# Performance work log

Measured on AMD Instinct MI355X. Metric: run time of the kernel, lower is better.

The kernel has to match this reference:

```python
import jax, jax.numpy as jnp
import numpy as np

B, T, E, H, V = 64, 512, 512, 512, 50000

def setup_inputs() -> dict:
    key = jax.random.key(0)
    ks = jax.random.split(key, 8)
    x = jax.random.randint(ks[0], (B, T), 0, V)
    h0 = jax.random.normal(ks[1], (B, H), jnp.float32) * 0.1
    c0 = jax.random.normal(ks[2], (B, H), jnp.float32) * 0.1
    emb = jax.random.normal(ks[3], (V, E), jnp.float32) * 0.02
    emb = emb.at[0].set(0.0)  # padding_idx=0
    s_i = 1.0 / np.sqrt(H)
    W_ih = jax.random.uniform(ks[4], (4 * H, E), jnp.float32, -s_i, s_i)
    W_hh = jax.random.uniform(ks[5], (4 * H, H), jnp.float32, -s_i, s_i)
    b_ih = jax.random.uniform(ks[6], (4 * H,), jnp.float32, -s_i, s_i)
    b_hh = jax.random.uniform(ks[7], (4 * H,), jnp.float32, -s_i, s_i)
    return {"x": x, "h0": h0, "c0": c0, "emb": emb,
            "W_ih": W_ih, "W_hh": W_hh, "b_ih": b_ih, "b_hh": b_hh}

def reference(x, h0, c0, emb, W_ih, W_hh, b_ih, b_hh):
    # embedding lookup (option 'a'): [B, T, E]
    xs = emb[x]
    # precompute input-to-gate projections for all timesteps: [B, T, 4H]
    pre = jnp.einsum('bte,ge->btg', xs, W_ih) + b_ih + b_hh
    pre_t = jnp.swapaxes(pre, 0, 1)  # [T, B, 4H]

    def step(carry, p_t):
        h, c = carry
        gates = p_t + h @ W_hh.T  # [B, 4H]
        i, f, g, o = jnp.split(gates, 4, axis=-1)
        i = jax.nn.sigmoid(i)
        f = jax.nn.sigmoid(f)
        g = jnp.tanh(g)
        o = jax.nn.sigmoid(o)
        c_new = f * c + i * g
        h_new = o * jnp.tanh(c_new)
        return (h_new, c_new), h_new

    _, hs = jax.lax.scan(step, (h0, c0), pre_t)  # hs: [T, B, H]
    # original stacks per-batch lists of per-timestep hidden states -> [B, T, H]
    return jnp.swapaxes(hs, 0, 1)
```

## Files before the change

kernel.cpp:

```cpp
#include <hip/hip_runtime.h>
#include <stdint.h>

typedef __attribute__((ext_vector_type(8))) short short8;
typedef __attribute__((ext_vector_type(4))) short short4_;
typedef __attribute__((ext_vector_type(4))) float f4;
typedef __attribute__((ext_vector_type(4))) uint32_t u32x4;

#define B_ 64
#define T_ 512
#define E_ 512
#define H_ 512
#define GH 2048

static __device__ __forceinline__ uint16_t f2bf(float f) {
  uint32_t u = __builtin_bit_cast(uint32_t, f);
  uint32_t r = (u + 0x7FFFu + ((u >> 16) & 1u)) >> 16;
  return (uint16_t)r;
}
static __device__ __forceinline__ float bf2f(uint16_t b) {
  return __builtin_bit_cast(float, (uint32_t)b << 16);
}
static __device__ __forceinline__ float sigmoidf_(float x) {
  return 1.0f / (1.0f + __expf(-x));
}
static __device__ __forceinline__ float tanhf_(float x) {
  float e = __expf(-2.0f * fabsf(x));
  float t = (1.0f - e) / (1.0f + e);
  return __builtin_copysignf(t, x);
}

static __device__ __forceinline__ u32x4 ld_flag4_cc(const int* p) {
  u32x4 v;
  asm volatile("global_load_dwordx4 %0, %1, off sc0 sc1\n\ts_waitcnt vmcnt(0)"
               : "=v"(v) : "v"(p) : "memory");
  return v;
}
static __device__ __forceinline__ void ld_x4_cc(u32x4* d, const void* p) {
  asm volatile("global_load_dwordx4 %0, %1, off sc0 sc1" : "=v"(*d) : "v"(p));
}
static __device__ __forceinline__ void st_u32_cc(uint32_t* p, uint32_t v) {
  asm volatile("global_store_dword %0, %1, off sc0 sc1" :: "v"(p), "v"(v) : "memory");
}
static __device__ __forceinline__ void st_flag_cc(int* p, int v) {
  asm volatile("global_store_dword %0, %1, off sc0 sc1" :: "v"(p), "v"(v) : "memory");
}

__global__ void k_prep(const float* __restrict__ Whh, uint16_t* __restrict__ Whi_g,
                       uint16_t* __restrict__ Wlo_g) {
  int i = blockIdx.x * 256 + threadIdx.x;
  float w = Whh[i];
  uint16_t hi = f2bf(w);
  Whi_g[i] = hi;
  Wlo_g[i] = f2bf(w - bf2f(hi));
}

__global__ void k_init(const float* __restrict__ h0, uint32_t* __restrict__ hP0,
                       int* __restrict__ flags) {
  int i = blockIdx.x * 256 + threadIdx.x;
  if (i < B_ * H_) {
    float v = h0[i];
    uint16_t hi = f2bf(v);
    uint16_t lo = f2bf(v - bf2f(hi));
    hP0[i] = (uint32_t)hi | ((uint32_t)lo << 16);
  }
  if (i < 128) flags[i] = 0;
}

__launch_bounds__(256)
__global__ void k_pre(const int* __restrict__ x, const float* __restrict__ emb,
                      const float* __restrict__ Wih, const float* __restrict__ bih,
                      const float* __restrict__ bhh, float* __restrict__ pre2, int t0) {
  __shared__ uint16_t As[128 * 64];
  __shared__ uint16_t Bs[128 * 64];
  const int tid = threadIdx.x;
  const int tm = blockIdx.x >> 4;
  const int tn = blockIdx.x & 15;
  const int wid = tid >> 6, lane = tid & 63;
  const int wr = wid >> 1, wc = wid & 1;

  const int arow = tid >> 1;
  const int half = tid & 1;
  const int m = tm * 128 + arow;
  const int bb = m & 63;
  const int tt = t0 + (m >> 6);
  const int xid = x[bb * T_ + tt];
  const float* asrc = emb + (size_t)xid * E_ + half * 32;
  const float* bsrc = Wih + (size_t)(tn * 128 + arow) * E_ + half * 32;

  f4 acc[4][4];
#pragma unroll
  for (int a = 0; a < 4; ++a)
#pragma unroll
    for (int b = 0; b < 4; ++b) acc[a][b] = (f4){0.f, 0.f, 0.f, 0.f};

  for (int kk = 0; kk < 8; ++kk) {
    __syncthreads();
#pragma unroll
    for (int gi = 0; gi < 4; ++gi) {
      f4 a0 = *(const f4*)(asrc + kk * 64 + gi * 8);
      f4 a1 = *(const f4*)(asrc + kk * 64 + gi * 8 + 4);
      f4 b0 = *(const f4*)(bsrc + kk * 64 + gi * 8);
      f4 b1 = *(const f4*)(bsrc + kk * 64 + gi * 8 + 4);
      short8 va, vb;
#pragma unroll
      for (int j = 0; j < 4; ++j) {
        va[j] = (short)f2bf(a0[j]); va[4 + j] = (short)f2bf(a1[j]);
        vb[j] = (short)f2bf(b0[j]); vb[4 + j] = (short)f2bf(b1[j]);
      }
      int kq = half * 4 + gi;
      *(short8*)(As + arow * 64 + (kq ^ (arow & 7)) * 8) = va;
      *(short8*)(Bs + arow * 64 + (kq ^ (arow & 7)) * 8) = vb;
    }
    __syncthreads();
#pragma unroll
    for (int ks = 0; ks < 2; ++ks) {
      short8 af[4], bfr[4];
#pragma unroll
      for (int mi = 0; mi < 4; ++mi) {
        int row = wr * 64 + mi * 16 + (lane & 15);
        int kq = ks * 4 + (lane >> 4);
        af[mi] = *(const short8*)(As + row * 64 + (kq ^ (row & 7)) * 8);
      }
#pragma unroll
      for (int ni = 0; ni < 4; ++ni) {
        int row = wc * 64 + ni * 16 + (lane & 15);
        int kq = ks * 4 + (lane >> 4);
        bfr[ni] = *(const short8*)(Bs + row * 64 + (kq ^ (row & 7)) * 8);
      }
#pragma unroll
      for (int mi = 0; mi < 4; ++mi)
#pragma unroll
        for (int ni = 0; ni < 4; ++ni)
          acc[mi][ni] = __builtin_amdgcn_mfma_f32_16x16x32_bf16(af[mi], bfr[ni], acc[mi][ni], 0, 0, 0);
    }
  }
#pragma unroll
  for (int ni = 0; ni < 4; ++ni) {
    int n = tn * 128 + wc * 64 + ni * 16 + (lane & 15);
    float bias = bih[n] + bhh[n];
    int q = n >> 9, u = n & 511;
    int ug = u >> 4, uloc = u & 15;
    int gl = q * 16 + uloc;
#pragma unroll
    for (int mi = 0; mi < 4; ++mi) {
      int mrow = tm * 128 + wr * 64 + mi * 16 + (lane >> 4) * 4;
      int trel = mrow >> 6;
      int bbr = mrow & 63;
      f4 vst;
#pragma unroll
      for (int j = 0; j < 4; ++j) vst[j] = acc[mi][ni][j] + bias;
      float* dst = pre2 + (((size_t)trel * 32 + ug) * 4 + (bbr >> 4)) * 1024 + gl * 16 + (bbr & 15);
      *(f4*)dst = vst;
    }
  }
}

__launch_bounds__(256)
__global__ void k_lstm(const float* __restrict__ pre2, const uint16_t* __restrict__ Whi_g,
                       const uint16_t* __restrict__ Wlo_g, const float* __restrict__ c0,
                       float* __restrict__ out, uint32_t* __restrict__ hP0,
                       uint32_t* __restrict__ hP1, float* __restrict__ c_state,
                       int* __restrict__ flags, int t0, int TB) {
  extern __shared__ char smem[];
  uint16_t* WhiL = (uint16_t*)smem;
  uint16_t* WloL = (uint16_t*)(smem + 65536);
  uint16_t* Hh   = (uint16_t*)(smem + 131072);
  uint16_t* Hl   = (uint16_t*)(smem + 147456);

  const int tid = threadIdx.x;
  const int bg = blockIdx.x & 3;
  const int ug = blockIdx.x >> 2;
  const int wv = tid >> 6, lane = tid & 63;
  const int wi = lane & 15, hi4 = lane >> 4;
  const int q = wi & 3, v = wi >> 2;
  const int u = ug * 16 + wv * 4 + v;
  const int gl = q * 16 + wv * 4 + v;

  for (int it = 0; it < 16; ++it) {
    int gg = it * 256 + tid;
    int r = gg >> 6, kq = gg & 63;
    int grow = (r & 3) * 512 + ug * 16 + (r >> 4) * 4 + ((r >> 2) & 3);
    short8 whi = *(const short8*)(Whi_g + (size_t)grow * 512 + kq * 8);
    short8 wlo = *(const short8*)(Wlo_g + (size_t)grow * 512 + kq * 8);
    int kqs = (kq & ~7) | ((kq & 7) ^ (r & 7));
    *(short8*)(WhiL + r * 512 + kqs * 8) = whi;
    *(short8*)(WloL + r * 512 + kqs * 8) = wlo;
  }

  f4 c_reg;
  {
    const float* csrc = (t0 == 0) ? c0 : c_state;
    const int brow = bg * 16 + hi4 * 4;
#pragma unroll
    for (int j = 0; j < 4; ++j) c_reg[j] = csrc[(size_t)(brow + j) * H_ + u];
  }
  int* fbase = flags + bg * 32;
  int* myflag = fbase + ug;
  __syncthreads();

  for (int s = t0 + 1; s <= t0 + TB; ++s) {
    const uint32_t* hsrc = (((s - 1) & 1) ? hP1 : hP0) + (size_t)bg * 16 * 512;
    uint32_t* hdst = ((s & 1) ? hP1 : hP0) + (size_t)bg * 16 * 512;

    f4 accA, accB, accC;
    {
      const float* pblk = pre2 + (((size_t)(s - 1 - t0) * 32 + ug) * 4 + bg) * 1024;
      accA = *(const f4*)(pblk + gl * 16 + hi4 * 4);
      accB = (f4){0.f, 0.f, 0.f, 0.f};
      accC = accB;
    }

    {
      const int target = s - 1;
      int guard = 0;
      bool ok;
      do {
        ok = true;
        if (lane < 8) {
          u32x4 fv = ld_flag4_cc(fbase + lane * 4);
          ok = (int)fv[0] >= target && (int)fv[1] >= target &&
               (int)fv[2] >= target && (int)fv[3] >= target;
        }
        if (!__all(ok)) __builtin_amdgcn_s_sleep(1);
        if (++guard > (1 << 17)) break;
      } while (!__all(ok));
    }

    u32x4 d[8];
#pragma unroll
    for (int jj = 0; jj < 8; ++jj) {
      int local = jj * 64 + lane;
      int row = local >> 5;
      int u0v = wv * 128 + (local & 31) * 4;
      ld_x4_cc(&d[jj], hsrc + (size_t)row * 512 + u0v);
    }
    asm volatile("s_waitcnt vmcnt(0)" ::: "memory");
    __builtin_amdgcn_sched_barrier(0);
#pragma unroll
    for (int jj = 0; jj < 8; ++jj) asm volatile("" : "+v"(d[jj]));
#pragma unroll
    for (int jj = 0; jj < 8; ++jj) {
      int local = jj * 64 + lane;
      int row = local >> 5;
      int u0v = wv * 128 + (local & 31) * 4;
      int kq = u0v >> 3, half = (u0v >> 2) & 1;
      int kqs = (kq & ~7) | ((kq & 7) ^ (row & 7));
      short4_ hh, hl;
#pragma unroll
      for (int i = 0; i < 4; ++i) {
        hh[i] = (short)(d[jj][i] & 0xFFFFu);
        hl[i] = (short)(d[jj][i] >> 16);
      }
      *(short4_*)(Hh + row * 512 + kqs * 8 + half * 4) = hh;
      *(short4_*)(Hl + row * 512 + kqs * 8 + half * 4) = hl;
    }
    __syncthreads();

    const int br = wv * 16 + wi;
#pragma unroll 4
    for (int ks = 0; ks < 16; ++ks) {
      int kq = ks * 4 + hi4;
      int kqsA = (kq & ~7) | ((kq & 7) ^ (wi & 7));
      int kqsB = (kq & ~7) | ((kq & 7) ^ (br & 7));
      short8 ah = *(const short8*)(Hh + wi * 512 + kqsA * 8);
      short8 al = *(const short8*)(Hl + wi * 512 + kqsA * 8);
      short8 bh = *(const short8*)(WhiL + br * 512 + kqsB * 8);
      short8 bl = *(const short8*)(WloL + br * 512 + kqsB * 8);
      accA = __builtin_amdgcn_mfma_f32_16x16x32_bf16(ah, bh, accA, 0, 0, 0);
      accB = __builtin_amdgcn_mfma_f32_16x16x32_bf16(al, bh, accB, 0, 0, 0);
      accC = __builtin_amdgcn_mfma_f32_16x16x32_bf16(ah, bl, accC, 0, 0, 0);
    }

    const bool qb0 = (q & 1) != 0, qb1 = (q & 2) != 0;
    const int rowloc = hi4 * 4 + q;
    const int b = bg * 16 + rowloc;
    f4 a0;
#pragma unroll
    for (int j = 0; j < 4; ++j) a0[j] = accA[j] + accB[j] + accC[j];
    f4 x1, s1a, s1b, x2a, x2b;
#pragma unroll
    for (int j = 0; j < 4; ++j) x1[j] = __shfl_xor(a0[j], 1);
#pragma unroll
    for (int j = 0; j < 4; ++j) {
      s1a[j] = qb0 ? x1[j] : a0[j];
      s1b[j] = qb0 ? a0[j] : x1[j];
    }
#pragma unroll
    for (int j = 0; j < 4; ++j) {
      x2a[j] = __shfl_xor(s1a[j], 2);
      x2b[j] = __shfl_xor(s1b[j], 2);
    }
    f4 cn, hn;
#pragma unroll
    for (int j = 0; j < 4; ++j) {
      float gi = qb1 ? x2a[j] : s1a[j];
      float gg = qb1 ? s1a[j] : x2a[j];
      float gf = qb1 ? x2b[j] : s1b[j];
      float go = qb1 ? s1b[j] : x2b[j];
      float iv = sigmoidf_(gi);
      float fv = sigmoidf_(gf);
      float gv = tanhf_(gg);
      float ov = sigmoidf_(go);
      float c2 = fv * c_reg[j] + iv * gv;
      cn[j] = c2;
      hn[j] = ov * tanhf_(c2);
    }
    c_reg = cn;
    float s01 = qb0 ? hn[1] : hn[0];
    float s23 = qb0 ? hn[3] : hn[2];
    float hq = qb1 ? s23 : s01;

    uint16_t hhi = f2bf(hq);
    uint16_t hlo = f2bf(hq - bf2f(hhi));
    st_u32_cc(hdst + (size_t)rowloc * 512 + u, (uint32_t)hhi | ((uint32_t)hlo << 16));
    asm volatile("s_waitcnt vmcnt(0)" ::: "memory");
    __syncthreads();
    if (tid == 0) st_flag_cc(myflag, s);
    __builtin_nontemporal_store(hq, &out[(size_t)b * (T_ * H_) + (size_t)(s - 1) * H_ + u]);
  }

  {
    const bool qb0 = (q & 1) != 0, qb1 = (q & 2) != 0;
    const int b = bg * 16 + hi4 * 4 + q;
    float c01 = qb0 ? c_reg[1] : c_reg[0];
    float c23 = qb0 ? c_reg[3] : c_reg[2];
    c_state[(size_t)b * H_ + u] = qb1 ? c23 : c01;
  }
}

extern "C" void kernel_launch(void* const* d_in, const int* in_sizes, int n_in,
                              void* d_out, int out_size, void* d_ws, size_t ws_size,
                              hipStream_t stream) {
  (void)in_sizes; (void)n_in; (void)out_size;
  const int* x = (const int*)d_in[0];
  const float* h0 = (const float*)d_in[1];
  const float* c0 = (const float*)d_in[2];
  const float* emb = (const float*)d_in[3];
  const float* Wih = (const float*)d_in[4];
  const float* Whh = (const float*)d_in[5];
  const float* bih = (const float*)d_in[6];
  const float* bhh = (const float*)d_in[7];
  float* out = (float*)d_out;
  char* ws = (char*)d_ws;

  int* flags = (int*)ws;
  float* c_state = (float*)(ws + 4096);
  uint32_t* hP0 = (uint32_t*)(ws + 135168);
  uint32_t* hP1 = (uint32_t*)(ws + 266240);
  uint16_t* Whi_g = (uint16_t*)(ws + 397312);
  uint16_t* Wlo_g = (uint16_t*)(ws + 2494464);
  float* pre2 = (float*)(ws + 4591616);

  int TB = 512;
  while (TB > 2 && (size_t)4591616 + (size_t)TB * 524288 > ws_size) TB >>= 1;

  (void)hipFuncSetAttribute(reinterpret_cast<const void*>(k_lstm),
                            hipFuncAttributeMaxDynamicSharedMemorySize, 163840);

  k_prep<<<dim3(4096), dim3(256), 0, stream>>>(Whh, Whi_g, Wlo_g);
  k_init<<<dim3(128), dim3(256), 0, stream>>>(h0, hP0, flags);
  for (int t0 = 0; t0 < 512; t0 += TB) {
    k_pre<<<dim3((TB * 64 / 128) * 16), dim3(256), 0, stream>>>(x, emb, Wih, bih, bhh, pre2, t0);
    k_lstm<<<dim3(128), dim3(256), 163840, stream>>>(pre2, Whi_g, Wlo_g, c0, out, hP0, hP1,
                                                     c_state, flags, t0, TB);
  }
}
```

Baseline: 2.317 ms.

## Prefetch peer flags, split MFMA accumulators, use nontemporal pre-gate traffic

The recurrent LSTM kernel now loads peer step flags speculatively right after publishing its own h, alongside the existing vmcnt wait, so the next step's spin-wait often passes without a fresh global round trip. The K-loop is fully unrolled with two independent accumulator sets per product, which shortens the MFMA dependency chains on the serial critical path. Pre-gate stores and loads use nontemporal hints to reduce cache pollution. Risks include stale flag reads forcing a fallback poll, extra register pressure, and slightly different summation order.

```diff
diff --git a/kernel.cpp b/kernel.cpp
--- a/kernel.cpp
+++ b/kernel.cpp
@@ -150,7 +150,7 @@
 #pragma unroll
       for (int j = 0; j < 4; ++j) vst[j] = acc[mi][ni][j] + bias;
       float* dst = pre2 + (((size_t)trel * 32 + ug) * 4 + (bbr >> 4)) * 1024 + gl * 16 + (bbr & 15);
-      *(f4*)dst = vst;
+      __builtin_nontemporal_store(vst, (f4*)dst);
     }
   }
 }
@@ -196,6 +196,7 @@
   }
   int* fbase = flags + bg * 32;
   int* myflag = fbase + ug;
+  u32x4 fv0 = (u32x4){0, 0, 0, 0};
   __syncthreads();
 
   for (int s = t0 + 1; s <= t0 + TB; ++s) {
@@ -204,26 +205,30 @@
 
     f4 accA, accB, accC;
     {
-      const float* pblk = pre2 + (((size_t)(s - 1 - t0) * 32 + ug) * 4 + bg) * 1024;
-      accA = *(const f4*)(pblk + gl * 16 + hi4 * 4);
+      const f4* pp = (const f4*)(pre2 + (((size_t)(s - 1 - t0) * 32 + ug) * 4 + bg) * 1024 +
+                                 gl * 16 + hi4 * 4);
+      accA = __builtin_nontemporal_load(pp);
       accB = (f4){0.f, 0.f, 0.f, 0.f};
       accC = accB;
     }
 
     {
       const int target = s - 1;
+      bool ok = true;
+      if (lane < 8)
+        ok = (int)fv0[0] >= target && (int)fv0[1] >= target &&
+             (int)fv0[2] >= target && (int)fv0[3] >= target;
       int guard = 0;
-      bool ok;
-      do {
+      while (!__all(ok)) {
+        __builtin_amdgcn_s_sleep(1);
         ok = true;
         if (lane < 8) {
           u32x4 fv = ld_flag4_cc(fbase + lane * 4);
           ok = (int)fv[0] >= target && (int)fv[1] >= target &&
                (int)fv[2] >= target && (int)fv[3] >= target;
         }
-        if (!__all(ok)) __builtin_amdgcn_s_sleep(1);
         if (++guard > (1 << 17)) break;
-      } while (!__all(ok));
+      }
     }
 
     u32x4 d[8];
@@ -256,19 +261,30 @@
     }
     __syncthreads();
 
+    f4 accA2 = (f4){0.f, 0.f, 0.f, 0.f}, accB2 = accA2, accC2 = accA2;
     const int br = wv * 16 + wi;
-#pragma unroll 4
-    for (int ks = 0; ks < 16; ++ks) {
-      int kq = ks * 4 + hi4;
-      int kqsA = (kq & ~7) | ((kq & 7) ^ (wi & 7));
-      int kqsB = (kq & ~7) | ((kq & 7) ^ (br & 7));
-      short8 ah = *(const short8*)(Hh + wi * 512 + kqsA * 8);
-      short8 al = *(const short8*)(Hl + wi * 512 + kqsA * 8);
-      short8 bh = *(const short8*)(WhiL + br * 512 + kqsB * 8);
-      short8 bl = *(const short8*)(WloL + br * 512 + kqsB * 8);
-      accA = __builtin_amdgcn_mfma_f32_16x16x32_bf16(ah, bh, accA, 0, 0, 0);
-      accB = __builtin_amdgcn_mfma_f32_16x16x32_bf16(al, bh, accB, 0, 0, 0);
-      accC = __builtin_amdgcn_mfma_f32_16x16x32_bf16(ah, bl, accC, 0, 0, 0);
+#pragma unroll
+    for (int ks2 = 0; ks2 < 8; ++ks2) {
+#pragma unroll
+      for (int p = 0; p < 2; ++p) {
+        int ks = ks2 * 2 + p;
+        int kq = ks * 4 + hi4;
+        int kqsA = (kq & ~7) | ((kq & 7) ^ (wi & 7));
+        int kqsB = (kq & ~7) | ((kq & 7) ^ (br & 7));
+        short8 ah = *(const short8*)(Hh + wi * 512 + kqsA * 8);
+        short8 al = *(const short8*)(Hl + wi * 512 + kqsA * 8);
+        short8 bh = *(const short8*)(WhiL + br * 512 + kqsB * 8);
+        short8 bl = *(const short8*)(WloL + br * 512 + kqsB * 8);
+        if (p == 0) {
+          accA = __builtin_amdgcn_mfma_f32_16x16x32_bf16(ah, bh, accA, 0, 0, 0);
+          accB = __builtin_amdgcn_mfma_f32_16x16x32_bf16(al, bh, accB, 0, 0, 0);
+          accC = __builtin_amdgcn_mfma_f32_16x16x32_bf16(ah, bl, accC, 0, 0, 0);
+        } else {
+          accA2 = __builtin_amdgcn_mfma_f32_16x16x32_bf16(ah, bh, accA2, 0, 0, 0);
+          accB2 = __builtin_amdgcn_mfma_f32_16x16x32_bf16(al, bh, accB2, 0, 0, 0);
+          accC2 = __builtin_amdgcn_mfma_f32_16x16x32_bf16(ah, bl, accC2, 0, 0, 0);
+        }
+      }
     }
 
     const bool qb0 = (q & 1) != 0, qb1 = (q & 2) != 0;
@@ -276,7 +292,8 @@
     const int b = bg * 16 + rowloc;
     f4 a0;
 #pragma unroll
-    for (int j = 0; j < 4; ++j) a0[j] = accA[j] + accB[j] + accC[j];
+    for (int j = 0; j < 4; ++j)
+      a0[j] = (accA[j] + accA2[j]) + (accB[j] + accB2[j]) + (accC[j] + accC2[j]);
     f4 x1, s1a, s1b, x2a, x2b;
 #pragma unroll
     for (int j = 0; j < 4; ++j) x1[j] = __shfl_xor(a0[j], 1);
@@ -313,7 +330,10 @@
     uint16_t hhi = f2bf(hq);
     uint16_t hlo = f2bf(hq - bf2f(hhi));
     st_u32_cc(hdst + (size_t)rowloc * 512 + u, (uint32_t)hhi | ((uint32_t)hlo << 16));
+    if (lane < 8) ld_x4_cc(&fv0, fbase + lane * 4);
     asm volatile("s_waitcnt vmcnt(0)" ::: "memory");
+    __builtin_amdgcn_sched_barrier(0);
+    asm volatile("" : "+v"(fv0));
     __syncthreads();
     if (tid == 0) st_flag_cc(myflag, s);
     __builtin_nontemporal_store(hq, &out[(size_t)b * (T_ * H_) + (size_t)(s - 1) * H_ + u]);
```

New measurement: 2.300 ms. No clear change (-0.7%).
